# Optimization experiments

Measured on AMD Instinct MI355X. Metric: run time of the kernel, lower is better.

## Reference

```python
import jax, jax.numpy as jnp
import numpy as np

B, N, D, H = 4, 2048, 256, 4
HD = D // H


def _linear(x, W, b):
    return x @ W.T + b


def _rotate_half(x):
    # pairs (x0,x1) -> (-x1, x0)
    x1 = x[..., ::2]
    x2 = x[..., 1::2]
    return jnp.stack((-x2, x1), axis=-1).reshape(x.shape)


def _layernorm(x, g, b, eps=1e-5):
    m = jnp.mean(x, axis=-1, keepdims=True)
    v = jnp.mean((x - m) ** 2, axis=-1, keepdims=True)
    return (x - m) / jnp.sqrt(v + eps) * g + b


def _ffn(x, W1, b1, g, be, W2, b2):
    h = _linear(x, W1, b1)
    h = _layernorm(h, g, be)
    h = jax.nn.gelu(h, approximate=False)
    return _linear(h, W2, b2)


def _self_block(x, enc, Wqkv, bqkv, Wout, bout, W1, b1, g, be, W2, b2):
    Bq, Nq, _ = x.shape
    qkv = _linear(x, Wqkv, bqkv).reshape(Bq, Nq, H, HD, 3).transpose(0, 2, 1, 3, 4)  # [B,H,N,HD,3]
    q, k, v = qkv[..., 0], qkv[..., 1], qkv[..., 2]
    q = q * enc[0] + _rotate_half(q) * enc[1]
    k = k * enc[0] + _rotate_half(k) * enc[1]
    scale = HD ** -0.5
    sim = jnp.einsum('bhid,bhjd->bhij', q, k) * scale
    attn = jax.nn.softmax(sim, axis=-1)
    ctx = jnp.einsum('bhij,bhjd->bhid', attn, v)
    msg = _linear(ctx.transpose(0, 2, 1, 3).reshape(Bq, Nq, D), Wout, bout)
    return x + _ffn(jnp.concatenate([x, msg], axis=-1), W1, b1, g, be, W2, b2)


def _cross_block(x0, x1, Wqk, bqk, Wv, bv, Wo, bo, W1, b1, g, be, W2, b2):
    def heads(t):
        return t.reshape(t.shape[0], t.shape[1], H, HD).transpose(0, 2, 1, 3)  # [B,H,N,HD]
    qk0 = heads(_linear(x0, Wqk, bqk))
    qk1 = heads(_linear(x1, Wqk, bqk))
    v0 = heads(_linear(x0, Wv, bv))
    v1 = heads(_linear(x1, Wv, bv))
    s = (HD ** -0.5) ** 0.5
    qk0 = qk0 * s
    qk1 = qk1 * s
    sim = jnp.einsum('bhid,bhjd->bhij', qk0, qk1)
    attn01 = jax.nn.softmax(sim, axis=-1)   # over j (x1 tokens)
    attn10 = jax.nn.softmax(sim, axis=-2)   # over i (x0 tokens)
    m0 = jnp.einsum('bhij,bhjd->bhid', attn01, v1)
    m1 = jnp.einsum('bhij,bhid->bhjd', attn10, v0)
    def unheads(t):
        return t.transpose(0, 2, 1, 3).reshape(t.shape[0], t.shape[2], D)
    m0 = _linear(unheads(m0), Wo, bo)
    m1 = _linear(unheads(m1), Wo, bo)
    x0 = x0 + _ffn(jnp.concatenate([x0, m0], axis=-1), W1, b1, g, be, W2, b2)
    x1 = x1 + _ffn(jnp.concatenate([x1, m1], axis=-1), W1, b1, g, be, W2, b2)
    return x0, x1


def setup_inputs() -> dict:
    key = jax.random.key(0)
    ks = jax.random.split(key, 32)
    std = 0.05

    def rn(k, shape, s=std):
        return jax.random.normal(k, shape, dtype=jnp.float32) * s

    def enc(k):
        ang = jax.random.uniform(k, (B, 1, N, HD // 2), dtype=jnp.float32) * (2 * np.pi)
        cos = jnp.repeat(jnp.cos(ang), 2, axis=-1)
        sin = jnp.repeat(jnp.sin(ang), 2, axis=-1)
        return jnp.stack([cos, sin], axis=0)  # [2,B,1,N,HD]

    return {
        'desc0': rn(ks[0], (B, N, D), 1.0),
        'desc1': rn(ks[1], (B, N, D), 1.0),
        'enc0': enc(ks[2]),
        'enc1': enc(ks[3]),
        's_Wqkv': rn(ks[4], (3 * D, D)), 's_bqkv': jnp.zeros((3 * D,), jnp.float32),
        's_Wout': rn(ks[5], (D, D)), 's_bout': jnp.zeros((D,), jnp.float32),
        's_W1': rn(ks[6], (2 * D, 2 * D)), 's_b1': jnp.zeros((2 * D,), jnp.float32),
        's_g': jnp.ones((2 * D,), jnp.float32), 's_be': jnp.zeros((2 * D,), jnp.float32),
        's_W2': rn(ks[7], (D, 2 * D)), 's_b2': jnp.zeros((D,), jnp.float32),
        'c_Wqk': rn(ks[8], (D, D)), 'c_bqk': jnp.zeros((D,), jnp.float32),
        'c_Wv': rn(ks[9], (D, D)), 'c_bv': jnp.zeros((D,), jnp.float32),
        'c_Wo': rn(ks[10], (D, D)), 'c_bo': jnp.zeros((D,), jnp.float32),
        'c_W1': rn(ks[11], (2 * D, 2 * D)), 'c_b1': jnp.zeros((2 * D,), jnp.float32),
        'c_g': jnp.ones((2 * D,), jnp.float32), 'c_be': jnp.zeros((2 * D,), jnp.float32),
        'c_W2': rn(ks[12], (D, 2 * D)), 'c_b2': jnp.zeros((D,), jnp.float32),
    }


def reference(desc0, desc1, enc0, enc1,
              s_Wqkv, s_bqkv, s_Wout, s_bout, s_W1, s_b1, s_g, s_be, s_W2, s_b2,
              c_Wqk, c_bqk, c_Wv, c_bv, c_Wo, c_bo, c_W1, c_b1, c_g, c_be, c_W2, c_b2):
    d0 = _self_block(desc0, enc0, s_Wqkv, s_bqkv, s_Wout, s_bout, s_W1, s_b1, s_g, s_be, s_W2, s_b2)
    d1 = _self_block(desc1, enc1, s_Wqkv, s_bqkv, s_Wout, s_bout, s_W1, s_b1, s_g, s_be, s_W2, s_b2)
    return _cross_block(d0, d1, c_Wqk, c_bqk, c_Wv, c_bv, c_Wo, c_bo, c_W1, c_b1, c_g, c_be, c_W2, c_b2)
```

## Files before the change

### kernel.cpp

```cpp
#include <hip/hip_runtime.h>
#include <cstddef>

#define NTOK 2048
#define BDIM 4
#define DIM 256
#define NHEAD 4
#define MROWS 8192
#define M2 16384
#define NMu ((size_t)MROWS * DIM)

typedef unsigned short u16;
typedef __attribute__((ext_vector_type(8))) short short8;
typedef __attribute__((ext_vector_type(4))) float f32x4;

#if __has_builtin(__builtin_amdgcn_exp2f)
#define EXP2(x) __builtin_amdgcn_exp2f(x)
#else
#define EXP2(x) exp2f(x)
#endif

__device__ __forceinline__ u16 f2bf(float x) {
  union { float f; unsigned u; } c; c.f = x;
  unsigned r = c.u + 0x7FFFu + ((c.u >> 16) & 1u);
  return (u16)(r >> 16);
}
__device__ __forceinline__ float bf2f(u16 u) {
  union { unsigned u; float f; } c; c.u = ((unsigned)u) << 16;
  return c.f;
}

__device__ __forceinline__ void glds16(const void* g, void* l) {
  __builtin_amdgcn_global_load_lds(
      (const __attribute__((address_space(1))) unsigned int*)g,
      (__attribute__((address_space(3))) unsigned int*)l, 16, 0, 0);
}

__global__ __launch_bounds__(256) void gemm_bf16_kernel(
    const u16* __restrict__ A, int lda,
    const u16* __restrict__ A2, int lda2, int kSplit,
    const u16* __restrict__ W,
    const float* __restrict__ bias0, const float* __restrict__ bias1,
    int nsplit, float os0, float os1,
    u16* __restrict__ Yb0, int ldy0,
    u16* __restrict__ Yb1, int ldy1,
    int K)
{
  __shared__ u16 As[2 * 4096];
  __shared__ u16 Bs[2 * 4096];
  const int t = threadIdx.x;
  const int m0 = blockIdx.y * 128, n0 = blockIdx.x * 128;
  const int r4 = t >> 2, c8 = (t & 3) * 8;
  const int lane = t & 63, w = t >> 6;
  const int cl = lane & 15, quad = lane >> 4;
  const int wm = (w >> 1) * 64, wn = (w & 1) * 64;

  f32x4 acc[4][4];
#pragma unroll
  for (int i = 0; i < 4; ++i)
#pragma unroll
    for (int j = 0; j < 4; ++j) acc[i][j] = (f32x4){0.f, 0.f, 0.f, 0.f};

  for (int k0 = 0; k0 < K; k0 += 64) {
    const u16* Ab; int la; int kk;
    if (k0 < kSplit) { Ab = A; la = lda; kk = k0; }
    else             { Ab = A2; la = lda2; kk = k0 - kSplit; }
    const u16* ag = Ab + (size_t)(m0 + r4) * la + kk + c8;
    const u16* bg = W + (size_t)(n0 + r4) * K + k0 + c8;
    __syncthreads();
#pragma unroll
    for (int kh = 0; kh < 2; ++kh) {
      glds16(ag + kh * 32, &As[kh * 4096 + t * 8]);
      glds16(ag + (size_t)64 * la + kh * 32, &As[kh * 4096 + 2048 + t * 8]);
      glds16(bg + kh * 32, &Bs[kh * 4096 + t * 8]);
      glds16(bg + (size_t)64 * K + kh * 32, &Bs[kh * 4096 + 2048 + t * 8]);
    }
    __syncthreads();

#pragma unroll
    for (int kh = 0; kh < 2; ++kh) {
      short8 af[4], bfr[4];
#pragma unroll
      for (int i = 0; i < 4; ++i)
        af[i] = *(const short8*)&As[kh * 4096 + (wm + i * 16 + cl) * 32 + quad * 8];
#pragma unroll
      for (int i = 0; i < 4; ++i)
        bfr[i] = *(const short8*)&Bs[kh * 4096 + (wn + i * 16 + cl) * 32 + quad * 8];
#pragma unroll
      for (int mt = 0; mt < 4; ++mt)
#pragma unroll
        for (int nt = 0; nt < 4; ++nt)
          acc[mt][nt] = __builtin_amdgcn_mfma_f32_16x16x32_bf16(
              af[mt], bfr[nt], acc[mt][nt], 0, 0, 0);
    }
  }

#pragma unroll
  for (int mt = 0; mt < 4; ++mt)
#pragma unroll
    for (int nt = 0; nt < 4; ++nt) {
      const int colg = n0 + wn + nt * 16 + cl;
      const bool first = colg < nsplit;
      const int c2 = first ? colg : colg - nsplit;
      const float bs = first ? bias0[c2] : bias1[c2];
      const float os = first ? os0 : os1;
      u16* yb = first ? Yb0 : Yb1;
      const int ly = first ? ldy0 : ldy1;
#pragma unroll
      for (int r = 0; r < 4; ++r) {
        const int rowg = m0 + wm + mt * 16 + quad * 4 + r;
        yb[(size_t)rowg * ly + c2] = f2bf((acc[mt][nt][r] + bs) * os);
      }
    }
}

__global__ __launch_bounds__(256) void gemm64_kernel(
    const u16* __restrict__ A, int lda,
    const u16* __restrict__ W,
    const float* __restrict__ bias,
    const u16* __restrict__ resb, int ldrb,
    float* __restrict__ Yf, int ldyf,
    u16* __restrict__ Yb, int ldyb,
    int K)
{
  __shared__ u16 As[2 * 2048];
  __shared__ u16 Bs[2 * 2048];
  const int t = threadIdx.x;
  const int m0 = blockIdx.y * 64, n0 = blockIdx.x * 64;
  const int r8 = t >> 2, c8 = (t & 3) * 8;
  const int lane = t & 63, w = t >> 6;
  const int cl = lane & 15, quad = lane >> 4;
  const int wm = (w >> 1) * 32, wn = (w & 1) * 32;

  f32x4 acc[2][2];
#pragma unroll
  for (int i = 0; i < 2; ++i)
#pragma unroll
    for (int j = 0; j < 2; ++j) acc[i][j] = (f32x4){0.f, 0.f, 0.f, 0.f};

  for (int k0 = 0; k0 < K; k0 += 64) {
    const u16* ag = A + (size_t)(m0 + r8) * lda + k0 + c8;
    const u16* bg = W + (size_t)(n0 + r8) * K + k0 + c8;
    __syncthreads();
#pragma unroll
    for (int kh = 0; kh < 2; ++kh) {
      glds16(ag + kh * 32, &As[kh * 2048 + t * 8]);
      glds16(bg + kh * 32, &Bs[kh * 2048 + t * 8]);
    }
    __syncthreads();

#pragma unroll
    for (int kh = 0; kh < 2; ++kh) {
      short8 af[2], bfr[2];
#pragma unroll
      for (int i = 0; i < 2; ++i)
        af[i] = *(const short8*)&As[kh * 2048 + (wm + i * 16 + cl) * 32 + quad * 8];
#pragma unroll
      for (int j = 0; j < 2; ++j)
        bfr[j] = *(const short8*)&Bs[kh * 2048 + (wn + j * 16 + cl) * 32 + quad * 8];
#pragma unroll
      for (int mt = 0; mt < 2; ++mt)
#pragma unroll
        for (int nt = 0; nt < 2; ++nt)
          acc[mt][nt] = __builtin_amdgcn_mfma_f32_16x16x32_bf16(
              af[mt], bfr[nt], acc[mt][nt], 0, 0, 0);
    }
  }

#pragma unroll
  for (int mt = 0; mt < 2; ++mt)
#pragma unroll
    for (int nt = 0; nt < 2; ++nt) {
      const int colg = n0 + wn + nt * 16 + cl;
      const float bs = bias[colg];
#pragma unroll
      for (int r = 0; r < 4; ++r) {
        const int rowg = m0 + wm + mt * 16 + quad * 4 + r;
        float v = acc[mt][nt][r] + bs;
        if (resb) v += bf2f(resb[(size_t)rowg * ldrb + colg]);
        if (Yf) Yf[(size_t)rowg * ldyf + colg] = v;
        if (Yb) Yb[(size_t)rowg * ldyb + colg] = f2bf(v);
      }
    }
}

__global__ __launch_bounds__(256) void wfuse_kernel(
    const float* __restrict__ W1, const float* __restrict__ Wo,
    const float* __restrict__ b1, const float* __restrict__ bo,
    const float* __restrict__ cW1, const float* __restrict__ cWo,
    const float* __restrict__ cb1, const float* __restrict__ cbo,
    u16* __restrict__ W1f, u16* __restrict__ cW1f,
    float* __restrict__ b1f, float* __restrict__ cb1f)
{
  const int n = blockIdx.x, sel = blockIdx.y;
  const float* Ws = sel ? cW1 : W1;
  const float* Wos = sel ? cWo : Wo;
  u16* out = sel ? cW1f : W1f;
  __shared__ float rowh[256];
  const int t = threadIdx.x;
  rowh[t] = Ws[(size_t)n * 512 + 256 + t];
  out[(size_t)n * 512 + t] = f2bf(Ws[(size_t)n * 512 + t]);
  __syncthreads();
  float acc = 0.f;
  for (int m = 0; m < 256; ++m) acc += rowh[m] * Wos[(size_t)m * 256 + t];
  out[(size_t)n * 512 + 256 + t] = f2bf(acc);
  if (t == 0) {
    const float* bos = sel ? cbo : bo;
    const float* b1s = sel ? cb1 : b1;
    float a = b1s[n];
    for (int m = 0; m < 256; ++m) a += rowh[m] * bos[m];
    (sel ? cb1f : b1f)[n] = a;
  }
}

__global__ __launch_bounds__(256) void rope_repack_kernel(
    const u16* __restrict__ qkv, const float* __restrict__ enc0,
    const float* __restrict__ enc1,
    u16* __restrict__ Q, u16* __restrict__ K, u16* __restrict__ V)
{
  const int idx = blockIdx.x * blockDim.x + threadIdx.x;
  const int i = idx & 31;
  const int h = (idx >> 5) & 3;
  const int m = idx >> 7;
  const int half = m >> 13;
  const int lm = m & (MROWS - 1);
  const float* enc = half ? enc1 : enc0;
  const u16* src = qkv + (size_t)m * 768 + h * 192 + i * 6;
  const unsigned a0 = *(const unsigned*)(src);
  const unsigned a1 = *(const unsigned*)(src + 2);
  const unsigned a2 = *(const unsigned*)(src + 4);
  const float q0 = bf2f((u16)a0), k0 = bf2f((u16)(a0 >> 16));
  const float v0 = bf2f((u16)a1), q1 = bf2f((u16)(a1 >> 16));
  const float k1 = bf2f((u16)a2), v1 = bf2f((u16)(a2 >> 16));
  const float c = enc[(size_t)lm * 64 + 2 * i];
  const float s = enc[(size_t)MROWS * 64 + (size_t)lm * 64 + 2 * i];
  const float QSC = 0.18033688011112042f;
  const size_t o = (size_t)m * 256 + h * 64 + 2 * i;
  *(unsigned*)(Q + o) = (unsigned)f2bf((q0 * c - q1 * s) * QSC) |
                        ((unsigned)f2bf((q1 * c + q0 * s) * QSC) << 16);
  *(unsigned*)(K + o) = (unsigned)f2bf(k0 * c - k1 * s) |
                        ((unsigned)f2bf(k1 * c + k0 * s) << 16);
  *(unsigned*)(V + o) = (unsigned)f2bf(v0) | ((unsigned)f2bf(v1) << 16);
}

__global__ __launch_bounds__(256) void transpose_v_kernel(
    const u16* __restrict__ in, u16* __restrict__ out)
{
  __shared__ u16 Tl[64][72];
  const int bz = blockIdx.z, h = blockIdx.y;
  const int n0 = blockIdx.x * 64;
  const int t = threadIdx.x;
  {
    const int row = t >> 2, c16 = (t & 3) * 16;
    const u16* src = in + (size_t)(bz * NTOK + n0 + row) * 256 + h * 64 + c16;
    *(uint4*)&Tl[row][c16] = *(const uint4*)src;
    *(uint4*)&Tl[row][c16 + 8] = *(const uint4*)(src + 8);
  }
  __syncthreads();
  const int d = t >> 2, qr = t & 3;
  union { u16 u[16]; uint4 v[2]; } pk;
#pragma unroll
  for (int j = 0; j < 16; ++j) pk.u[j] = Tl[qr * 16 + j][d];
  u16* dst = out + ((size_t)((bz * NHEAD + h) * 64 + d)) * NTOK + n0 + qr * 16;
  *(uint4*)dst = pk.v[0];
  *(uint4*)(dst + 8) = pk.v[1];
}

__global__ __launch_bounds__(256, 4) void attn3_kernel(
    const u16* __restrict__ Qb, const u16* __restrict__ Kb,
    const u16* __restrict__ Vtb,
    u16* __restrict__ Po, float* __restrict__ Pl,
    int cross)
{
  __shared__ u16 Ks[64 * 72];
  __shared__ u16 Vs[64 * 72];
  __shared__ u16 QPs[128 * 72];
  const int y = blockIdx.y, z = blockIdx.z;
  const int h2 = y >> 4, b = (y >> 2) & 3, h = y & 3;
  const int kh = cross ? (1 - h2) : h2;
  const int qrowbase = (h2 * 4 + b) * NTOK;
  const int krowbase = (kh * 4 + b) * NTOK + z * 1024;
  const int vz = kh * 4 + b;
  const int n0 = blockIdx.x * 128;
  const int t = threadIdx.x, lane = t & 63, w = t >> 6;
  const int cl = lane & 15, quad = lane >> 4;

  {
    const int row = t >> 1, c32 = (t & 1) * 32;
    const u16* src = Qb + (size_t)(qrowbase + n0 + row) * 256 + h * 64 + c32;
    uint4 v0 = *(const uint4*)src;
    uint4 v1 = *(const uint4*)(src + 8);
    uint4 v2 = *(const uint4*)(src + 16);
    uint4 v3 = *(const uint4*)(src + 24);
    u16* d = &QPs[row * 72 + c32];
    *(uint4*)d = v0; *(uint4*)(d + 8) = v1;
    *(uint4*)(d + 16) = v2; *(uint4*)(d + 24) = v3;
  }
  __syncthreads();
  const int q0 = w * 32;
  short8 bq[2][2];
#pragma unroll
  for (int c = 0; c < 2; ++c) {
    bq[c][0] = *(const short8*)&QPs[(q0 + c * 16 + cl) * 72 + quad * 8];
    bq[c][1] = *(const short8*)&QPs[(q0 + c * 16 + cl) * 72 + quad * 8 + 32];
  }

  float l_r[2] = {0.f, 0.f};
  f32x4 o[2][4];
#pragma unroll
  for (int c = 0; c < 2; ++c)
#pragma unroll
    for (int i = 0; i < 4; ++i) o[c][i] = (f32x4){0.f, 0.f, 0.f, 0.f};

  const int srow = t >> 2, sc16 = (t & 3) * 16;
  const u16* Kg = Kb + (size_t)(krowbase + srow) * 256 + h * 64 + sc16;
  const u16* Vg = Vtb + ((size_t)(vz * NHEAD + h) * 64 + srow) * NTOK + z * 1024 + sc16;
  uint4 ka0 = *(const uint4*)Kg, ka1 = *(const uint4*)(Kg + 8);
  uint4 va0 = *(const uint4*)Vg, va1 = *(const uint4*)(Vg + 8);

  for (int tile = 0; tile < 16; ++tile) {
    __syncthreads();
    *(uint4*)&Ks[srow * 72 + sc16] = ka0;
    *(uint4*)&Ks[srow * 72 + sc16 + 8] = ka1;
    *(uint4*)&Vs[srow * 72 + sc16] = va0;
    *(uint4*)&Vs[srow * 72 + sc16 + 8] = va1;
    __syncthreads();
    if (tile < 15) {
      Kg += 64 * 256; Vg += 64;
      ka0 = *(const uint4*)Kg; ka1 = *(const uint4*)(Kg + 8);
      va0 = *(const uint4*)Vg; va1 = *(const uint4*)(Vg + 8);
    }

    f32x4 sf[2][4];
#pragma unroll
    for (int kb = 0; kb < 4; ++kb) {
      short8 ak0 = *(const short8*)&Ks[(kb * 16 + cl) * 72 + quad * 8];
      short8 ak1 = *(const short8*)&Ks[(kb * 16 + cl) * 72 + quad * 8 + 32];
#pragma unroll
      for (int c = 0; c < 2; ++c) {
        f32x4 acc = (f32x4){0.f, 0.f, 0.f, 0.f};
        acc = __builtin_amdgcn_mfma_f32_16x16x32_bf16(ak0, bq[c][0], acc, 0, 0, 0);
        acc = __builtin_amdgcn_mfma_f32_16x16x32_bf16(ak1, bq[c][1], acc, 0, 0, 0);
        sf[c][kb] = acc;
      }
    }

#pragma unroll
    for (int c = 0; c < 2; ++c) {
      float rs = 0.f;
#pragma unroll
      for (int kb = 0; kb < 4; ++kb)
#pragma unroll
        for (int r = 0; r < 4; ++r) {
          const float p = EXP2(sf[c][kb][r]);
          sf[c][kb][r] = p; rs += p;
        }
      rs += __shfl_xor(rs, 16);
      rs += __shfl_xor(rs, 32);
      l_r[c] += rs;
#pragma unroll
      for (int kb = 0; kb < 4; ++kb) {
        unsigned d0 = __builtin_amdgcn_perm(__float_as_uint(sf[c][kb][1]),
                                            __float_as_uint(sf[c][kb][0]), 0x07060302u);
        unsigned d1 = __builtin_amdgcn_perm(__float_as_uint(sf[c][kb][3]),
                                            __float_as_uint(sf[c][kb][2]), 0x07060302u);
        uint2 pk; pk.x = d0; pk.y = d1;
        *(uint2*)&QPs[(q0 + c * 16 + cl) * 72 + kb * 16 + quad * 4] = pk;
      }
    }

    short8 bp[2][2];
#pragma unroll
    for (int c = 0; c < 2; ++c) {
      bp[c][0] = *(const short8*)&QPs[(q0 + c * 16 + cl) * 72 + quad * 8];
      bp[c][1] = *(const short8*)&QPs[(q0 + c * 16 + cl) * 72 + quad * 8 + 32];
    }
#pragma unroll
    for (int db = 0; db < 4; ++db) {
      short8 av0 = *(const short8*)&Vs[(db * 16 + cl) * 72 + quad * 8];
      short8 av1 = *(const short8*)&Vs[(db * 16 + cl) * 72 + quad * 8 + 32];
#pragma unroll
      for (int c = 0; c < 2; ++c) {
        o[c][db] = __builtin_amdgcn_mfma_f32_16x16x32_bf16(av0, bp[c][0], o[c][db], 0, 0, 0);
        o[c][db] = __builtin_amdgcn_mfma_f32_16x16x32_bf16(av1, bp[c][1], o[c][db], 0, 0, 0);
      }
    }
  }

#pragma unroll
  for (int c = 0; c < 2; ++c) {
    const int rp = z * 65536 + y * 2048 + n0 + q0 + c * 16 + cl;
#pragma unroll
    for (int db = 0; db < 4; ++db) {
      ushort4 st;
      st.x = f2bf(o[c][db][0]); st.y = f2bf(o[c][db][1]);
      st.z = f2bf(o[c][db][2]); st.w = f2bf(o[c][db][3]);
      *(ushort4*)(Po + (size_t)rp * 64 + db * 16 + quad * 4) = st;
    }
    if (quad == 0) { Pl[rp] = l_r[c]; }
  }
}

__global__ __launch_bounds__(256) void attn_combine_kernel(
    const u16* __restrict__ Po, const float* __restrict__ Pl,
    u16* __restrict__ Ou)
{
  const int rowi = blockIdx.x * 4 + (threadIdx.x >> 6);
  const int lane = threadIdx.x & 63;
  const float l0 = Pl[rowi], l1 = Pl[65536 + rowi];
  const float inv = 1.f / (l0 + l1);
  const float o0 = bf2f(Po[(size_t)rowi * 64 + lane]);
  const float o1 = bf2f(Po[(size_t)65536 * 64 + (size_t)rowi * 64 + lane]);
  const float val = (o0 + o1) * inv;
  const int y = rowi >> 11, q = rowi & 2047;
  const int bz = y >> 2, h = y & 3;
  Ou[(size_t)(bz * NTOK + q) * 256 + h * 64 + lane] = f2bf(val);
}

__global__ __launch_bounds__(256) void ln_gelu_kernel(
    const u16* __restrict__ Hm, const float* __restrict__ g,
    const float* __restrict__ be, u16* __restrict__ out)
{
  const int rowi = blockIdx.x * 4 + (threadIdx.x >> 6);
  const int lane = threadIdx.x & 63;
  const u16* row = Hm + (size_t)rowi * 512 + lane * 8;
  u16* orow = out + (size_t)rowi * 512 + lane * 8;
  uint4 raw = *(const uint4*)row;
  float x[8];
  const unsigned* rw = (const unsigned*)&raw;
#pragma unroll
  for (int i = 0; i < 4; ++i) {
    x[2 * i]     = bf2f((u16)rw[i]);
    x[2 * i + 1] = bf2f((u16)(rw[i] >> 16));
  }
  float s = 0.f;
#pragma unroll
  for (int i = 0; i < 8; ++i) s += x[i];
#pragma unroll
  for (int off = 32; off; off >>= 1) s += __shfl_xor(s, off);
  const float mean = s * (1.f / 512.f);
  float s2 = 0.f;
#pragma unroll
  for (int i = 0; i < 8; ++i) { const float d = x[i] - mean; s2 += d * d; }
#pragma unroll
  for (int off = 32; off; off >>= 1) s2 += __shfl_xor(s2, off);
  const float rstd = rsqrtf(s2 * (1.f / 512.f) + 1e-5f);
  unsigned ov[4];
#pragma unroll
  for (int i = 0; i < 4; ++i) {
    const int c = lane * 8 + 2 * i;
    const float y0 = (x[2 * i] - mean) * rstd * g[c] + be[c];
    const float y1 = (x[2 * i + 1] - mean) * rstd * g[c + 1] + be[c + 1];
    const float g0 = 0.5f * y0 * (1.f + erff(y0 * 0.70710678118654752f));
    const float g1 = 0.5f * y1 * (1.f + erff(y1 * 0.70710678118654752f));
    ov[i] = (unsigned)f2bf(g0) | ((unsigned)f2bf(g1) << 16);
  }
  *(uint4*)orow = *(uint4*)ov;
}

__global__ __launch_bounds__(256) void pack_all_kernel(
    const float* w0, const float* w1, const float* w2, const float* w3,
    const float* w4, const float* d0, const float* d1,
    u16* __restrict__ wb, u16* __restrict__ descb)
{
  const size_t idx4 = ((size_t)blockIdx.x * 256 + threadIdx.x) * 4;
  const float* src; u16* dst; size_t off;
  if (idx4 < 589824) {
    off = idx4; dst = wb + idx4;
    if      (idx4 < 196608) { src = w0; }
    else if (idx4 < 327680) { src = w1; off -= 196608; }
    else if (idx4 < 393216) { src = w2; off -= 327680; }
    else if (idx4 < 458752) { src = w3; off -= 393216; }
    else                    { src = w4; off -= 458752; }
  } else {
    size_t o = idx4 - 589824;
    dst = descb + o;
    if (o < NMu) { src = d0; off = o; }
    else         { src = d1; off = o - NMu; }
  }
  float4 v = *(const float4*)(src + off);
  ushort4 ov;
  ov.x = f2bf(v.x); ov.y = f2bf(v.y); ov.z = f2bf(v.z); ov.w = f2bf(v.w);
  *(ushort4*)dst = ov;
}

extern "C" void kernel_launch(void* const* d_in, const int* in_sizes, int n_in,
                              void* d_out, int out_size, void* d_ws, size_t ws_size,
                              hipStream_t stream) {
  const float* desc0  = (const float*)d_in[0];
  const float* desc1  = (const float*)d_in[1];
  const float* enc0   = (const float*)d_in[2];
  const float* enc1   = (const float*)d_in[3];
  const float* s_Wqkv = (const float*)d_in[4];
  const float* s_bqkv = (const float*)d_in[5];
  const float* s_Wout = (const float*)d_in[6];
  const float* s_bout = (const float*)d_in[7];
  const float* s_W1   = (const float*)d_in[8];
  const float* s_b1   = (const float*)d_in[9];
  const float* s_g    = (const float*)d_in[10];
  const float* s_be   = (const float*)d_in[11];
  const float* s_W2   = (const float*)d_in[12];
  const float* s_b2   = (const float*)d_in[13];
  const float* c_Wqk  = (const float*)d_in[14];
  const float* c_bqk  = (const float*)d_in[15];
  const float* c_Wv   = (const float*)d_in[16];
  const float* c_bv   = (const float*)d_in[17];
  const float* c_Wo   = (const float*)d_in[18];
  const float* c_bo   = (const float*)d_in[19];
  const float* c_W1   = (const float*)d_in[20];
  const float* c_b1   = (const float*)d_in[21];
  const float* c_g    = (const float*)d_in[22];
  const float* c_be   = (const float*)d_in[23];
  const float* c_W2   = (const float*)d_in[24];
  const float* c_b2   = (const float*)d_in[25];

  u16* U = (u16*)d_ws;
  u16* descb = U + 0 * NMu;
  u16* qkvb  = U + 2 * NMu;
  u16* ctxb  = U + 2 * NMu;
  u16* Qu    = U + 8 * NMu;
  u16* Ku    = U + 10 * NMu;
  u16* Vu    = U + 12 * NMu;
  u16* Vt    = U + 14 * NMu;
  u16* hbufb = U + 12 * NMu;
  u16* Po    = U + 16 * NMu;
  u16* hb2   = U + 16 * NMu;
  float* Pl  = (float*)(U + 20 * NMu);
  float* b1f = Pl + 2 * 65536;
  float* cb1f = b1f + 512;
  u16* s_b   = U + 21 * NMu;
  u16* wb    = U + 23 * NMu;

  u16* Wqkvb = wb;
  u16* W2b   = wb + 196608;
  u16* cQKVb = wb + 327680;
  u16* cW2b  = wb + 458752;
  u16* W1f   = wb + 589824;
  u16* cW1f  = wb + 851968;

  float* outf = (float*)d_out;

  const dim3 attn_grid(NTOK / 128, 32, 2);
  const dim3 tv_grid(NTOK / 64, NHEAD, 8);
  const int rope_blocks = (M2 * 128) / 256;
  const int lng_blocks  = M2 / 4;
  const int comb_blocks = 65536 / 4;
  const float csc = 0.42466090014400953f;

  hipLaunchKernelGGL(pack_all_kernel, dim3(4672), dim3(256), 0, stream,
                     s_Wqkv, s_W2, c_Wqk, c_Wv, c_W2, desc0, desc1, wb, descb);
  hipLaunchKernelGGL(wfuse_kernel, dim3(512, 2), dim3(256), 0, stream,
                     s_W1, s_Wout, s_b1, s_bout, c_W1, c_Wo, c_b1, c_bo,
                     W1f, cW1f, b1f, cb1f);

  hipLaunchKernelGGL(gemm_bf16_kernel, dim3(6, 128), dim3(256), 0, stream,
                     descb, 256, (const u16*)nullptr, 0, 1 << 30, Wqkvb,
                     s_bqkv, (const float*)nullptr, 1 << 30, 1.f, 1.f,
                     qkvb, 768, (u16*)nullptr, 0, 256);
  hipLaunchKernelGGL(rope_repack_kernel, dim3(rope_blocks), dim3(256), 0, stream,
                     qkvb, enc0, enc1, Qu, Ku, Vu);
  hipLaunchKernelGGL(transpose_v_kernel, tv_grid, dim3(256), 0, stream, Vu, Vt);
  hipLaunchKernelGGL(attn3_kernel, attn_grid, dim3(256), 0, stream,
                     Qu, Ku, Vt, Po, Pl, 0);
  hipLaunchKernelGGL(attn_combine_kernel, dim3(comb_blocks), dim3(256), 0, stream,
                     Po, Pl, ctxb);
  hipLaunchKernelGGL(gemm_bf16_kernel, dim3(4, 128), dim3(256), 0, stream,
                     descb, 256, ctxb, 256, 256, W1f,
                     b1f, (const float*)nullptr, 1 << 30, 1.f, 1.f,
                     hbufb, 512, (u16*)nullptr, 0, 512);
  hipLaunchKernelGGL(ln_gelu_kernel, dim3(lng_blocks), dim3(256), 0, stream,
                     hbufb, s_g, s_be, hb2);
  hipLaunchKernelGGL(gemm64_kernel, dim3(4, 256), dim3(256), 0, stream,
                     hb2, 512, W2b, s_b2, descb, 256,
                     (float*)nullptr, 0, s_b, 256, 512);

  u16* qkb = Qu;
  u16* vb  = Ku;
  hipLaunchKernelGGL(gemm_bf16_kernel, dim3(4, 128), dim3(256), 0, stream,
                     s_b, 256, (const u16*)nullptr, 0, 1 << 30, cQKVb,
                     c_bqk, c_bv, 256, csc, 1.f,
                     qkb, 256, vb, 256, 256);
  hipLaunchKernelGGL(transpose_v_kernel, tv_grid, dim3(256), 0, stream, vb, Vt);
  hipLaunchKernelGGL(attn3_kernel, attn_grid, dim3(256), 0, stream,
                     qkb, qkb, Vt, Po, Pl, 1);
  hipLaunchKernelGGL(attn_combine_kernel, dim3(comb_blocks), dim3(256), 0, stream,
                     Po, Pl, ctxb);
  hipLaunchKernelGGL(gemm_bf16_kernel, dim3(4, 128), dim3(256), 0, stream,
                     s_b, 256, ctxb, 256, 256, cW1f,
                     cb1f, (const float*)nullptr, 1 << 30, 1.f, 1.f,
                     hbufb, 512, (u16*)nullptr, 0, 512);
  hipLaunchKernelGGL(ln_gelu_kernel, dim3(lng_blocks), dim3(256), 0, stream,
                     hbufb, c_g, c_be, hb2);
  hipLaunchKernelGGL(gemm64_kernel, dim3(4, 256), dim3(256), 0, stream,
                     hb2, 512, cW2b, c_b2, s_b, 256,
                     outf, 256, (u16*)nullptr, 0, 512);
}
```

Before: 396.9 us.

## Drop split-K attention and combine pass; double-buffer K/V tiles in LDS

The attention kernel now handles the full 2048-key range in one block instead of two halves, normalises in place, and writes directly to the context buffer. This removes the separate combine kernel and its partial-output round trip through memory. K/V tiles are double-buffered in shared memory with one barrier per tile, and the block index is remapped to group heads. The grid shrinks from 1024 to 512 blocks, each twice as long, with the occupancy hint lowered from 4 to 2, which may reduce parallelism on the GPU.

```diff
diff --git a/kernel.cpp b/kernel.cpp
--- a/kernel.cpp
+++ b/kernel.cpp
@@ -265,22 +265,24 @@
   *(uint4*)(dst + 8) = pk.v[1];
 }
 
-__global__ __launch_bounds__(256, 4) void attn3_kernel(
+__global__ __launch_bounds__(256, 2) void attn4_kernel(
     const u16* __restrict__ Qb, const u16* __restrict__ Kb,
-    const u16* __restrict__ Vtb,
-    u16* __restrict__ Po, float* __restrict__ Pl,
-    int cross)
-{
-  __shared__ u16 Ks[64 * 72];
-  __shared__ u16 Vs[64 * 72];
+    const u16* __restrict__ Vtb, u16* __restrict__ Ou, int cross)
+{
+  __shared__ u16 Ks[2][64 * 72];
+  __shared__ u16 Vs[2][64 * 72];
   __shared__ u16 QPs[128 * 72];
-  const int y = blockIdx.y, z = blockIdx.z;
+
+  const int hw = blockIdx.x;
+  const int li = hw >> 3;
+  const int y  = (hw & 7) * 4 + (li >> 4);
+  const int n0 = (li & 15) * 128;
+
   const int h2 = y >> 4, b = (y >> 2) & 3, h = y & 3;
   const int kh = cross ? (1 - h2) : h2;
   const int qrowbase = (h2 * 4 + b) * NTOK;
-  const int krowbase = (kh * 4 + b) * NTOK + z * 1024;
+  const int krowbase = (kh * 4 + b) * NTOK;
   const int vz = kh * 4 + b;
-  const int n0 = blockIdx.x * 128;
   const int t = threadIdx.x, lane = t & 63, w = t >> 6;
   const int cl = lane & 15, quad = lane >> 4;
 
@@ -295,7 +297,6 @@
     *(uint4*)d = v0; *(uint4*)(d + 8) = v1;
     *(uint4*)(d + 16) = v2; *(uint4*)(d + 24) = v3;
   }
-  __syncthreads();
   const int q0 = w * 32;
   short8 bq[2][2];
 #pragma unroll
@@ -313,34 +314,42 @@
 
   const int srow = t >> 2, sc16 = (t & 3) * 16;
   const u16* Kg = Kb + (size_t)(krowbase + srow) * 256 + h * 64 + sc16;
-  const u16* Vg = Vtb + ((size_t)(vz * NHEAD + h) * 64 + srow) * NTOK + z * 1024 + sc16;
+  const u16* Vg = Vtb + ((size_t)(vz * NHEAD + h) * 64 + srow) * NTOK + sc16;
+
   uint4 ka0 = *(const uint4*)Kg, ka1 = *(const uint4*)(Kg + 8);
   uint4 va0 = *(const uint4*)Vg, va1 = *(const uint4*)(Vg + 8);
-
-  for (int tile = 0; tile < 16; ++tile) {
-    __syncthreads();
-    *(uint4*)&Ks[srow * 72 + sc16] = ka0;
-    *(uint4*)&Ks[srow * 72 + sc16 + 8] = ka1;
-    *(uint4*)&Vs[srow * 72 + sc16] = va0;
-    *(uint4*)&Vs[srow * 72 + sc16 + 8] = va1;
-    __syncthreads();
-    if (tile < 15) {
-      Kg += 64 * 256; Vg += 64;
-      ka0 = *(const uint4*)Kg; ka1 = *(const uint4*)(Kg + 8);
-      va0 = *(const uint4*)Vg; va1 = *(const uint4*)(Vg + 8);
-    }
+  *(uint4*)&Ks[0][srow * 72 + sc16] = ka0;
+  *(uint4*)&Ks[0][srow * 72 + sc16 + 8] = ka1;
+  *(uint4*)&Vs[0][srow * 72 + sc16] = va0;
+  *(uint4*)&Vs[0][srow * 72 + sc16 + 8] = va1;
+  Kg += 64 * 256; Vg += 64;
+  ka0 = *(const uint4*)Kg; ka1 = *(const uint4*)(Kg + 8);
+  va0 = *(const uint4*)Vg; va1 = *(const uint4*)(Vg + 8);
+  __syncthreads();
+
+  for (int tile = 0; tile < 32; ++tile) {
+    const int cur = tile & 1, nxt = cur ^ 1;
 
     f32x4 sf[2][4];
 #pragma unroll
     for (int kb = 0; kb < 4; ++kb) {
-      short8 ak0 = *(const short8*)&Ks[(kb * 16 + cl) * 72 + quad * 8];
-      short8 ak1 = *(const short8*)&Ks[(kb * 16 + cl) * 72 + quad * 8 + 32];
+      short8 ak0 = *(const short8*)&Ks[cur][(kb * 16 + cl) * 72 + quad * 8];
+      short8 ak1 = *(const short8*)&Ks[cur][(kb * 16 + cl) * 72 + quad * 8 + 32];
 #pragma unroll
       for (int c = 0; c < 2; ++c) {
         f32x4 acc = (f32x4){0.f, 0.f, 0.f, 0.f};
         acc = __builtin_amdgcn_mfma_f32_16x16x32_bf16(ak0, bq[c][0], acc, 0, 0, 0);
         acc = __builtin_amdgcn_mfma_f32_16x16x32_bf16(ak1, bq[c][1], acc, 0, 0, 0);
         sf[c][kb] = acc;
+      }
+    }
+
+    if (tile < 31) {
+      *(uint4*)&Ks[nxt][srow * 72 + sc16] = ka0;
+      *(uint4*)&Ks[nxt][srow * 72 + sc16 + 8] = ka1;
+      if (tile < 30) {
+        Kg += 64 * 256;
+        ka0 = *(const uint4*)Kg; ka1 = *(const uint4*)(Kg + 8);
       }
     }
 
@@ -376,44 +385,38 @@
     }
 #pragma unroll
     for (int db = 0; db < 4; ++db) {
-      short8 av0 = *(const short8*)&Vs[(db * 16 + cl) * 72 + quad * 8];
-      short8 av1 = *(const short8*)&Vs[(db * 16 + cl) * 72 + quad * 8 + 32];
+      short8 av0 = *(const short8*)&Vs[cur][(db * 16 + cl) * 72 + quad * 8];
+      short8 av1 = *(const short8*)&Vs[cur][(db * 16 + cl) * 72 + quad * 8 + 32];
 #pragma unroll
       for (int c = 0; c < 2; ++c) {
         o[c][db] = __builtin_amdgcn_mfma_f32_16x16x32_bf16(av0, bp[c][0], o[c][db], 0, 0, 0);
         o[c][db] = __builtin_amdgcn_mfma_f32_16x16x32_bf16(av1, bp[c][1], o[c][db], 0, 0, 0);
       }
     }
+
+    if (tile < 31) {
+      *(uint4*)&Vs[nxt][srow * 72 + sc16] = va0;
+      *(uint4*)&Vs[nxt][srow * 72 + sc16 + 8] = va1;
+      if (tile < 30) {
+        Vg += 64;
+        va0 = *(const uint4*)Vg; va1 = *(const uint4*)(Vg + 8);
+      }
+    }
+    __syncthreads();
   }
 
 #pragma unroll
   for (int c = 0; c < 2; ++c) {
-    const int rp = z * 65536 + y * 2048 + n0 + q0 + c * 16 + cl;
+    const float inv = 1.f / l_r[c];
+    const size_t rowo = (size_t)(qrowbase + n0 + q0 + c * 16 + cl) * 256 + h * 64;
 #pragma unroll
     for (int db = 0; db < 4; ++db) {
       ushort4 st;
-      st.x = f2bf(o[c][db][0]); st.y = f2bf(o[c][db][1]);
-      st.z = f2bf(o[c][db][2]); st.w = f2bf(o[c][db][3]);
-      *(ushort4*)(Po + (size_t)rp * 64 + db * 16 + quad * 4) = st;
-    }
-    if (quad == 0) { Pl[rp] = l_r[c]; }
-  }
-}
-
-__global__ __launch_bounds__(256) void attn_combine_kernel(
-    const u16* __restrict__ Po, const float* __restrict__ Pl,
-    u16* __restrict__ Ou)
-{
-  const int rowi = blockIdx.x * 4 + (threadIdx.x >> 6);
-  const int lane = threadIdx.x & 63;
-  const float l0 = Pl[rowi], l1 = Pl[65536 + rowi];
-  const float inv = 1.f / (l0 + l1);
-  const float o0 = bf2f(Po[(size_t)rowi * 64 + lane]);
-  const float o1 = bf2f(Po[(size_t)65536 * 64 + (size_t)rowi * 64 + lane]);
-  const float val = (o0 + o1) * inv;
-  const int y = rowi >> 11, q = rowi & 2047;
-  const int bz = y >> 2, h = y & 3;
-  Ou[(size_t)(bz * NTOK + q) * 256 + h * 64 + lane] = f2bf(val);
+      st.x = f2bf(o[c][db][0] * inv); st.y = f2bf(o[c][db][1] * inv);
+      st.z = f2bf(o[c][db][2] * inv); st.w = f2bf(o[c][db][3] * inv);
+      *(ushort4*)(Ou + rowo + db * 16 + quad * 4) = st;
+    }
+  }
 }
 
 __global__ __launch_bounds__(256) void ln_gelu_kernel(
@@ -522,10 +525,8 @@
   u16* Vu    = U + 12 * NMu;
   u16* Vt    = U + 14 * NMu;
   u16* hbufb = U + 12 * NMu;
-  u16* Po    = U + 16 * NMu;
   u16* hb2   = U + 16 * NMu;
-  float* Pl  = (float*)(U + 20 * NMu);
-  float* b1f = Pl + 2 * 65536;
+  float* b1f = (float*)(U + 20 * NMu);
   float* cb1f = b1f + 512;
   u16* s_b   = U + 21 * NMu;
   u16* wb    = U + 23 * NMu;
@@ -539,11 +540,9 @@
 
   float* outf = (float*)d_out;
 
-  const dim3 attn_grid(NTOK / 128, 32, 2);
   const dim3 tv_grid(NTOK / 64, NHEAD, 8);
   const int rope_blocks = (M2 * 128) / 256;
   const int lng_blocks  = M2 / 4;
-  const int comb_blocks = 65536 / 4;
   const float csc = 0.42466090014400953f;
 
   hipLaunchKernelGGL(pack_all_kernel, dim3(4672), dim3(256), 0, stream,
@@ -559,10 +558,8 @@
   hipLaunchKernelGGL(rope_repack_kernel, dim3(rope_blocks), dim3(256), 0, stream,
                      qkvb, enc0, enc1, Qu, Ku, Vu);
   hipLaunchKernelGGL(transpose_v_kernel, tv_grid, dim3(256), 0, stream, Vu, Vt);
-  hipLaunchKernelGGL(attn3_kernel, attn_grid, dim3(256), 0, stream,
-                     Qu, Ku, Vt, Po, Pl, 0);
-  hipLaunchKernelGGL(attn_combine_kernel, dim3(comb_blocks), dim3(256), 0, stream,
-                     Po, Pl, ctxb);
+  hipLaunchKernelGGL(attn4_kernel, dim3(512), dim3(256), 0, stream,
+                     Qu, Ku, Vt, ctxb, 0);
   hipLaunchKernelGGL(gemm_bf16_kernel, dim3(4, 128), dim3(256), 0, stream,
                      descb, 256, ctxb, 256, 256, W1f,
                      b1f, (const float*)nullptr, 1 << 30, 1.f, 1.f,
@@ -580,10 +577,8 @@
                      c_bqk, c_bv, 256, csc, 1.f,
                      qkb, 256, vb, 256, 256);
   hipLaunchKernelGGL(transpose_v_kernel, tv_grid, dim3(256), 0, stream, vb, Vt);
-  hipLaunchKernelGGL(attn3_kernel, attn_grid, dim3(256), 0, stream,
-                     qkb, qkb, Vt, Po, Pl, 1);
-  hipLaunchKernelGGL(attn_combine_kernel, dim3(comb_blocks), dim3(256), 0, stream,
-                     Po, Pl, ctxb);
+  hipLaunchKernelGGL(attn4_kernel, dim3(512), dim3(256), 0, stream,
+                     qkb, qkb, Vt, ctxb, 1);
   hipLaunchKernelGGL(gemm_bf16_kernel, dim3(4, 128), dim3(256), 0, stream,
                      s_b, 256, ctxb, 256, 256, cW1f,
                      cb1f, (const float*)nullptr, 1 << 30, 1.f, 1.f,
```

Result: no change. 390.2 us (-1.7%).
